# Kernel optimization log

Measured on AMD Instinct MI355X. Metric: run time of the kernel, lower is better.

Reference implementation:

```python
import jax, jax.numpy as jnp
import numpy as np
from jax.scipy.special import erfc

CUTOFF = 10.0   # real-space cutoff (Angstrom)
ALPHA = 0.3     # Ewald splitting parameter (1/Angstrom)
KMAX = 8        # max integer k-index per dimension
N_ATOMS = 4096
BOX = 40.0      # cubic box edge (Angstrom)


def setup_inputs() -> dict:
    key = jax.random.key(0)
    kp, kq = jax.random.split(key)
    positions = jax.random.uniform(kp, (N_ATOMS, 3), dtype=jnp.float32) * BOX
    charges = jax.random.normal(kq, (N_ATOMS,), dtype=jnp.float32)
    charges = charges - charges.mean()  # enforce charge neutrality
    cell = jnp.eye(3, dtype=jnp.float32) * BOX  # row-vector lattice
    return {"positions": positions, "charges": charges, "cell": cell}


def _kvectors(kmax):
    # static integer grid (-kmax..kmax)^3 \\ {0}, built with numpy at trace time
    n = np.arange(-kmax, kmax + 1)
    grid = np.stack(np.meshgrid(n, n, n, indexing="ij"), axis=-1).reshape(-1, 3)
    grid = grid[np.any(grid != 0, axis=-1)]
    return jnp.asarray(grid, dtype=jnp.float32)  # [Nk, 3]


def _ewald(positions, charges, cell, cutoff, alpha, kmax):
    N = positions.shape[0]
    inv_cell = jnp.linalg.inv(cell)

    # ---- real-space sum: 0.5 * sum_{i!=j, r<rc} q_i q_j erfc(a r)/r (min image)
    rij = positions[:, None, :] - positions[None, :, :]          # [N,N,3]
    frac = rij @ inv_cell
    rij = (frac - jnp.round(frac)) @ cell                        # minimum image
    r2 = jnp.sum(rij * rij, axis=-1)                             # [N,N]
    eye = jnp.eye(N, dtype=bool)
    r = jnp.sqrt(jnp.where(eye, 1.0, r2))                        # safe sqrt on diag
    pair_mask = (~eye) & (r2 < cutoff * cutoff)
    qq = charges[:, None] * charges[None, :]
    e_real = 0.5 * jnp.sum(jnp.where(pair_mask, qq * erfc(alpha * r) / r, 0.0))

    # ---- reciprocal-space sum: (2pi/V) sum_k exp(-k^2/4a^2)/k^2 |S(k)|^2
    recip = 2.0 * jnp.pi * inv_cell.T                            # reciprocal lattice rows
    kvecs = _kvectors(kmax) @ recip                              # [Nk,3]
    k2 = jnp.sum(kvecs * kvecs, axis=-1)                         # [Nk]
    phase = positions @ kvecs.T                                  # [N,Nk]
    s_re = charges @ jnp.cos(phase)                              # [Nk]
    s_im = charges @ jnp.sin(phase)                              # [Nk]
    vol = jnp.abs(jnp.linalg.det(cell))
    coeff = jnp.exp(-k2 / (4.0 * alpha * alpha)) / k2
    e_recip = (2.0 * jnp.pi / vol) * jnp.sum(coeff * (s_re * s_re + s_im * s_im))

    # ---- self-energy correction
    e_self = -(alpha / jnp.sqrt(jnp.pi)) * jnp.sum(charges * charges)

    return e_real + e_recip + e_self


def reference(positions, charges, cell):
    return _ewald(positions, charges, cell, CUTOFF, ALPHA, KMAX)
```

## Files before the change

kernel.cpp:

```cpp
#include <hip/hip_runtime.h>
#include <math.h>

#define ALPHA 0.3f
#define KMAX 8
#define KDIM 17
#define KD2 (KDIM*KDIM)
#define NK_FULL (KDIM*KDIM*KDIM - 1)
#define NK_HALF (NK_FULL/2)
#define RECIP_KB ((NK_HALF + 255)/256)
#define KPAD (RECIP_KB*256)
#define RECIP_CHUNKS 16
#define TWO_PI 6.28318530717958647692f

#define SELF_COEF (-0.16925687506432687f)
#define INV_4A2 (1.0f/(4.0f*ALPHA*ALPHA))
#define C1A (0.3275911f*ALPHA)
#define NA2 (-(ALPHA*ALPHA))

#define ITILE 256
#define JTILE 32

__device__ __forceinline__ void invert3x3(const float* __restrict__ c, float inv[9], float* det_out) {
    float a00=c[0],a01=c[1],a02=c[2];
    float a10=c[3],a11=c[4],a12=c[5];
    float a20=c[6],a21=c[7],a22=c[8];
    float c00 =  a11*a22 - a12*a21;
    float c01 = -(a10*a22 - a12*a20);
    float c02 =  a10*a21 - a11*a20;
    float det = a00*c00 + a01*c01 + a02*c02;
    float id = 1.0f/det;
    inv[0] =  c00*id;
    inv[1] = -(a01*a22 - a02*a21)*id;
    inv[2] =  (a01*a12 - a02*a11)*id;
    inv[3] =  c01*id;
    inv[4] =  (a00*a22 - a02*a20)*id;
    inv[5] = -(a00*a12 - a02*a10)*id;
    inv[6] =  c02*id;
    inv[7] = -(a00*a21 - a01*a20)*id;
    inv[8] =  (a00*a11 - a01*a10)*id;
    *det_out = det;
}

__device__ __forceinline__ float erfc_a(float r, float r2) {
    float t = __builtin_amdgcn_rcpf(fmaf(C1A, r, 1.0f));
    float p = t * fmaf(t, fmaf(t, fmaf(t, fmaf(t, 1.061405429f, -1.453152027f),
                       1.421413741f), -0.284496736f), 0.254829592f);
    return p * __expf(NA2 * r2);
}

__device__ __forceinline__ float block_reduce(float v) {
    for (int o = 32; o > 0; o >>= 1) v += __shfl_down(v, o, 64);
    __shared__ float smem[4];
    int lane = threadIdx.x & 63, wid = threadIdx.x >> 6;
    if (lane == 0) smem[wid] = v;
    __syncthreads();
    int nw = blockDim.x >> 6;
    v = ((int)threadIdx.x < nw) ? smem[threadIdx.x] : 0.0f;
    if (wid == 0) {
        for (int o = 4; o > 0; o >>= 1) v += __shfl_down(v, o, 64);
    }
    return v;
}

__global__ __launch_bounds__(256) void fused_kernel(const float* __restrict__ pos,
                                                    const float* __restrict__ q,
                                                    const float* __restrict__ cell,
                                                    float* __restrict__ spart,
                                                    float* __restrict__ rpart,
                                                    int N, int nb_recip) {
    __shared__ float4 tile[256];
    float inv[9]; float det;
    invert3x3(cell, inv, &det);
    bool ortho = (cell[1]==0.f) & (cell[2]==0.f) & (cell[3]==0.f) &
                 (cell[5]==0.f) & (cell[6]==0.f) & (cell[7]==0.f);

    int bid = blockIdx.x;
    int tid = threadIdx.x;

    if (bid < nb_recip) {
        int kb    = bid % RECIP_KB;
        int chunk = bid / RECIP_KB;
        int k = kb * 256 + tid;
        bool kvalid = (k < NK_HALF);
        int kk = kvalid ? k : 0;
        float kx = (float)(kk / KD2 - KMAX);
        float ky = (float)((kk / KDIM) % KDIM - KMAX);
        float kz = (float)(kk % KDIM - KMAX);

        int per = (N + RECIP_CHUNKS - 1) / RECIP_CHUNKS;
        int a0 = chunk * per;
        int a1 = min(N, a0 + per);

        float sre = 0.0f, sim = 0.0f;
        for (int base = a0; base < a1; base += 256) {
            int cnt = min(256, a1 - base);
            __syncthreads();
            if (tid < cnt) {
                int a = base + tid;
                float x = pos[3*a], y = pos[3*a+1], z = pos[3*a+2];
                float wx, wy, wz;
                if (ortho) { wx = x*inv[0]; wy = y*inv[4]; wz = z*inv[8]; }
                else {
                    wx = inv[0]*x + inv[3]*y + inv[6]*z;
                    wy = inv[1]*x + inv[4]*y + inv[7]*z;
                    wz = inv[2]*x + inv[5]*y + inv[8]*z;
                }
                tile[tid] = make_float4(wx, wy, wz, q[a]);
            }
            __syncthreads();
            #pragma unroll 4
            for (int t = 0; t < cnt; ++t) {
                float4 w = tile[t];
                float ph = fmaf(kx, w.x, fmaf(ky, w.y, kz * w.z));
                ph -= rintf(ph);
                sre = fmaf(w.w, __builtin_amdgcn_cosf(ph), sre);
                sim = fmaf(w.w, __builtin_amdgcn_sinf(ph), sim);
            }
        }
        spart[(size_t)(chunk*2    ) * KPAD + k] = kvalid ? sre : 0.0f;
        spart[(size_t)(chunk*2 + 1) * KPAD + k] = kvalid ? sim : 0.0f;
    } else {
        int rbid = bid - nb_recip;
        int bi = 0, acc = 0;
        for (;;) {
            int up = min(N, (bi + 1) * ITILE);
            int nc = (up + JTILE - 1) / JTILE;
            if (rbid < acc + nc) break;
            acc += nc; ++bi;
        }
        int bj = rbid - acc;

        float c0 = cell[0], c4 = cell[4], c8 = cell[8];
        float c1 = cell[1], c2 = cell[2], c3 = cell[3];
        float c5 = cell[5], c6 = cell[6], c7 = cell[7];

        int ibase = bi * ITILE;
        int i = ibase + tid;
        bool ivalid = (i < N);
        float xi = 0.f, yi = 0.f, zi = 0.f, qi = 0.f;
        if (ivalid) { xi = pos[3*i]; yi = pos[3*i+1]; zi = pos[3*i+2]; qi = q[i]; }

        int jbase = bj * JTILE;
        int jcount = min(JTILE, N - jbase);
        if (tid < jcount) {
            int j = jbase + tid;
            tile[tid] = make_float4(pos[3*j], pos[3*j+1], pos[3*j+2], q[j]);
        }
        __syncthreads();

        bool full = (jbase + JTILE <= ibase) && (ibase + ITILE <= N) && (jcount == JTILE);

        float acc_e = 0.0f;
        if (ortho) {
            float i0 = inv[0], i4 = inv[4], i8 = inv[8];
            if (full) {
                #pragma unroll 8
                for (int t = 0; t < JTILE; ++t) {
                    float4 p = tile[t];
                    float dx = xi - p.x, dy = yi - p.y, dz = zi - p.z;
                    float rx = fmaf(-c0, rintf(dx * i0), dx);
                    float ry = fmaf(-c4, rintf(dy * i4), dy);
                    float rz = fmaf(-c8, rintf(dz * i8), dz);
                    float r2 = fmaf(rx, rx, fmaf(ry, ry, rz * rz));
                    float rinv = __builtin_amdgcn_rsqf(r2);
                    float r = r2 * rinv;
                    acc_e = fmaf(p.w * rinv, erfc_a(r, r2), acc_e);
                }
            } else {
                #pragma unroll 8
                for (int t = 0; t < jcount; ++t) {
                    float4 p = tile[t];
                    float dx = xi - p.x, dy = yi - p.y, dz = zi - p.z;
                    float rx = fmaf(-c0, rintf(dx * i0), dx);
                    float ry = fmaf(-c4, rintf(dy * i4), dy);
                    float rz = fmaf(-c8, rintf(dz * i8), dz);
                    float r2 = fmaf(rx, rx, fmaf(ry, ry, rz * rz));
                    float rinv = __builtin_amdgcn_rsqf(r2);
                    float r = r2 * rinv;
                    float val = p.w * rinv * erfc_a(r, r2);
                    bool ok = ivalid && ((jbase + t) < i);
                    acc_e += ok ? val : 0.0f;
                }
            }
        } else {
            #pragma unroll 4
            for (int t = 0; t < jcount; ++t) {
                float4 p = tile[t];
                float dx = xi - p.x, dy = yi - p.y, dz = zi - p.z;
                float fx = dx*inv[0] + dy*inv[3] + dz*inv[6];
                float fy = dx*inv[1] + dy*inv[4] + dz*inv[7];
                float fz = dx*inv[2] + dy*inv[5] + dz*inv[8];
                fx -= rintf(fx); fy -= rintf(fy); fz -= rintf(fz);
                float rx = fx*c0 + fy*c3 + fz*c6;
                float ry = fx*c1 + fy*c4 + fz*c7;
                float rz = fx*c2 + fy*c5 + fz*c8;
                float r2 = fmaf(rx, rx, fmaf(ry, ry, rz * rz));
                float rinv = __builtin_amdgcn_rsqf(r2);
                float r = r2 * rinv;
                float val = p.w * rinv * erfc_a(r, r2);
                bool ok = ivalid && ((jbase + t) < i);
                acc_e += ok ? val : 0.0f;
            }
        }
        acc_e *= qi;

        float s = block_reduce(acc_e);
        if (tid == 0) rpart[rbid] = s;
    }
}

__global__ __launch_bounds__(256) void finalize_kernel(const float* __restrict__ spart,
                                                       const float* __restrict__ rpart,
                                                       const float* __restrict__ q,
                                                       const float* __restrict__ cell,
                                                       float* __restrict__ e_out,
                                                       int N, int nb_real) {
    float inv[9]; float det;
    invert3x3(cell, inv, &det);
    float vol = fabsf(det);
    float pref = 2.0f * (TWO_PI / vol);
    int tid = threadIdx.x;

    float acc = 0.0f;
    for (int t = tid; t < NK_HALF; t += 256) {
        float sr = 0.0f, si = 0.0f;
        #pragma unroll
        for (int c = 0; c < RECIP_CHUNKS; ++c) {
            sr += spart[(size_t)(c*2    ) * KPAD + t];
            si += spart[(size_t)(c*2 + 1) * KPAD + t];
        }
        float nx = (float)(t / KD2 - KMAX);
        float ny = (float)((t / KDIM) % KDIM - KMAX);
        float nz = (float)(t % KDIM - KMAX);
        float kvx = TWO_PI * (nx*inv[0] + ny*inv[1] + nz*inv[2]);
        float kvy = TWO_PI * (nx*inv[3] + ny*inv[4] + nz*inv[5]);
        float kvz = TWO_PI * (nx*inv[6] + ny*inv[7] + nz*inv[8]);
        float k2 = fmaf(kvx, kvx, fmaf(kvy, kvy, kvz * kvz));
        float coeff = __expf(-k2 * INV_4A2) / k2;
        acc = fmaf(pref * coeff, fmaf(sr, sr, si * si), acc);
    }
    for (int t = tid; t < N; t += 256) {
        float qt = q[t];
        acc = fmaf(SELF_COEF * qt, qt, acc);
    }
    for (int t = tid; t < nb_real; t += 256) {
        acc += rpart[t];
    }
    float s = block_reduce(acc);
    if (tid == 0) e_out[0] = s;
}

extern "C" void kernel_launch(void* const* d_in, const int* in_sizes, int n_in,
                              void* d_out, int out_size, void* d_ws, size_t ws_size,
                              hipStream_t stream) {
    const float* pos  = (const float*)d_in[0];
    const float* q    = (const float*)d_in[1];
    const float* cell = (const float*)d_in[2];
    int N = in_sizes[1];
    float* e_out = (float*)d_out;
    float* spart = (float*)d_ws;
    float* rpart = spart + (size_t)RECIP_CHUNKS*2*KPAD;

    int nbi = (N + ITILE - 1) / ITILE;
    int nb_real = 0;
    for (int bi = 0; bi < nbi; ++bi) {
        int up = (N < (bi + 1) * ITILE) ? N : (bi + 1) * ITILE;
        nb_real += (up + JTILE - 1) / JTILE;
    }
    int nb_recip = RECIP_KB * RECIP_CHUNKS;

    fused_kernel<<<nb_recip + nb_real, 256, 0, stream>>>(pos, q, cell, spart, rpart, N, nb_recip);

    finalize_kernel<<<1, 256, 0, stream>>>(spart, rpart, q, cell, e_out, N, nb_real);
}
```

Measured before the change: 80.13 us.

## Compute structure factors via kz recurrence and split real/recip kernels with atomics

The reciprocal sum now evaluates one sin/cos per (kx,ky) column and atom. It then walks the 17 kz values by complex multiplication with a precomputed per-atom exp(i*2pi*wz) phase factor, which replaces the per-k transcendental. Work is parallelized over atom chunks with atomic accumulation into S(k), and the fused kernel is split into separate real-space and reciprocal kernels. A memset is added, and the real-space partials are reduced with one float atomic per block. This trades transcendental throughput for register-heavy recurrences, many global atomics and extra launches, and it makes the float summation order nondeterministic.

```diff
diff --git a/kernel.cpp b/kernel.cpp
--- a/kernel.cpp
+++ b/kernel.cpp
@@ -4,13 +4,10 @@
 #define ALPHA 0.3f
 #define KMAX 8
 #define KDIM 17
-#define KD2 (KDIM*KDIM)
-#define NK_FULL (KDIM*KDIM*KDIM - 1)
-#define NK_HALF (NK_FULL/2)
-#define RECIP_KB ((NK_HALF + 255)/256)
-#define KPAD (RECIP_KB*256)
-#define RECIP_CHUNKS 16
 #define TWO_PI 6.28318530717958647692f
+
+#define NCOL 145
+#define NS (NCOL*17)
 
 #define SELF_COEF (-0.16925687506432687f)
 #define INV_4A2 (1.0f/(4.0f*ALPHA*ALPHA))
@@ -19,6 +16,8 @@
 
 #define ITILE 256
 #define JTILE 32
+#define RCHUNK 32
+#define RBLK 192
 
 __device__ __forceinline__ void invert3x3(const float* __restrict__ c, float inv[9], float* det_out) {
     float a00=c[0],a01=c[1],a02=c[2];
@@ -41,6 +40,12 @@
     *det_out = det;
 }
 
+__device__ __forceinline__ void col_to_k(int col, float* kx, float* ky) {
+    if (col < 136)      { *kx = (float)(col/17 - 8); *ky = (float)(col%17 - 8); }
+    else if (col < 144) { *kx = 0.f;                 *ky = (float)(col - 144);  }
+    else                { *kx = 0.f;                 *ky = 0.f; }
+}
+
 __device__ __forceinline__ float erfc_a(float r, float r2) {
     float t = __builtin_amdgcn_rcpf(fmaf(C1A, r, 1.0f));
     float p = t * fmaf(t, fmaf(t, fmaf(t, fmaf(t, 1.061405429f, -1.453152027f),
@@ -54,7 +59,7 @@
     int lane = threadIdx.x & 63, wid = threadIdx.x >> 6;
     if (lane == 0) smem[wid] = v;
     __syncthreads();
-    int nw = blockDim.x >> 6;
+    int nw = (blockDim.x + 63) >> 6;
     v = ((int)threadIdx.x < nw) ? smem[threadIdx.x] : 0.0f;
     if (wid == 0) {
         for (int o = 4; o > 0; o >>= 1) v += __shfl_down(v, o, 64);
@@ -62,138 +67,72 @@
     return v;
 }
 
-__global__ __launch_bounds__(256) void fused_kernel(const float* __restrict__ pos,
-                                                    const float* __restrict__ q,
-                                                    const float* __restrict__ cell,
-                                                    float* __restrict__ spart,
-                                                    float* __restrict__ rpart,
-                                                    int N, int nb_recip) {
-    __shared__ float4 tile[256];
+__global__ __launch_bounds__(256) void real_kernel(const float* __restrict__ pos,
+                                                   const float* __restrict__ q,
+                                                   const float* __restrict__ cell,
+                                                   float* __restrict__ ws_e,
+                                                   int N) {
+    __shared__ float4 tile[JTILE];
     float inv[9]; float det;
     invert3x3(cell, inv, &det);
     bool ortho = (cell[1]==0.f) & (cell[2]==0.f) & (cell[3]==0.f) &
                  (cell[5]==0.f) & (cell[6]==0.f) & (cell[7]==0.f);
 
-    int bid = blockIdx.x;
     int tid = threadIdx.x;
-
-    if (bid < nb_recip) {
-        int kb    = bid % RECIP_KB;
-        int chunk = bid / RECIP_KB;
-        int k = kb * 256 + tid;
-        bool kvalid = (k < NK_HALF);
-        int kk = kvalid ? k : 0;
-        float kx = (float)(kk / KD2 - KMAX);
-        float ky = (float)((kk / KDIM) % KDIM - KMAX);
-        float kz = (float)(kk % KDIM - KMAX);
-
-        int per = (N + RECIP_CHUNKS - 1) / RECIP_CHUNKS;
-        int a0 = chunk * per;
-        int a1 = min(N, a0 + per);
-
-        float sre = 0.0f, sim = 0.0f;
-        for (int base = a0; base < a1; base += 256) {
-            int cnt = min(256, a1 - base);
-            __syncthreads();
-            if (tid < cnt) {
-                int a = base + tid;
-                float x = pos[3*a], y = pos[3*a+1], z = pos[3*a+2];
-                float wx, wy, wz;
-                if (ortho) { wx = x*inv[0]; wy = y*inv[4]; wz = z*inv[8]; }
-                else {
-                    wx = inv[0]*x + inv[3]*y + inv[6]*z;
-                    wy = inv[1]*x + inv[4]*y + inv[7]*z;
-                    wz = inv[2]*x + inv[5]*y + inv[8]*z;
-                }
-                tile[tid] = make_float4(wx, wy, wz, q[a]);
-            }
-            __syncthreads();
-            #pragma unroll 4
-            for (int t = 0; t < cnt; ++t) {
-                float4 w = tile[t];
-                float ph = fmaf(kx, w.x, fmaf(ky, w.y, kz * w.z));
-                ph -= rintf(ph);
-                sre = fmaf(w.w, __builtin_amdgcn_cosf(ph), sre);
-                sim = fmaf(w.w, __builtin_amdgcn_sinf(ph), sim);
-            }
-        }
-        spart[(size_t)(chunk*2    ) * KPAD + k] = kvalid ? sre : 0.0f;
-        spart[(size_t)(chunk*2 + 1) * KPAD + k] = kvalid ? sim : 0.0f;
-    } else {
-        int rbid = bid - nb_recip;
-        int bi = 0, acc = 0;
-        for (;;) {
-            int up = min(N, (bi + 1) * ITILE);
-            int nc = (up + JTILE - 1) / JTILE;
-            if (rbid < acc + nc) break;
-            acc += nc; ++bi;
-        }
-        int bj = rbid - acc;
-
-        float c0 = cell[0], c4 = cell[4], c8 = cell[8];
-        float c1 = cell[1], c2 = cell[2], c3 = cell[3];
-        float c5 = cell[5], c6 = cell[6], c7 = cell[7];
-
-        int ibase = bi * ITILE;
-        int i = ibase + tid;
-        bool ivalid = (i < N);
-        float xi = 0.f, yi = 0.f, zi = 0.f, qi = 0.f;
-        if (ivalid) { xi = pos[3*i]; yi = pos[3*i+1]; zi = pos[3*i+2]; qi = q[i]; }
-
-        int jbase = bj * JTILE;
-        int jcount = min(JTILE, N - jbase);
-        if (tid < jcount) {
-            int j = jbase + tid;
-            tile[tid] = make_float4(pos[3*j], pos[3*j+1], pos[3*j+2], q[j]);
-        }
-        __syncthreads();
-
-        bool full = (jbase + JTILE <= ibase) && (ibase + ITILE <= N) && (jcount == JTILE);
-
-        float acc_e = 0.0f;
-        if (ortho) {
-            float i0 = inv[0], i4 = inv[4], i8 = inv[8];
-            if (full) {
-                #pragma unroll 8
-                for (int t = 0; t < JTILE; ++t) {
-                    float4 p = tile[t];
-                    float dx = xi - p.x, dy = yi - p.y, dz = zi - p.z;
-                    float rx = fmaf(-c0, rintf(dx * i0), dx);
-                    float ry = fmaf(-c4, rintf(dy * i4), dy);
-                    float rz = fmaf(-c8, rintf(dz * i8), dz);
-                    float r2 = fmaf(rx, rx, fmaf(ry, ry, rz * rz));
-                    float rinv = __builtin_amdgcn_rsqf(r2);
-                    float r = r2 * rinv;
-                    acc_e = fmaf(p.w * rinv, erfc_a(r, r2), acc_e);
-                }
-            } else {
-                #pragma unroll 8
-                for (int t = 0; t < jcount; ++t) {
-                    float4 p = tile[t];
-                    float dx = xi - p.x, dy = yi - p.y, dz = zi - p.z;
-                    float rx = fmaf(-c0, rintf(dx * i0), dx);
-                    float ry = fmaf(-c4, rintf(dy * i4), dy);
-                    float rz = fmaf(-c8, rintf(dz * i8), dz);
-                    float r2 = fmaf(rx, rx, fmaf(ry, ry, rz * rz));
-                    float rinv = __builtin_amdgcn_rsqf(r2);
-                    float r = r2 * rinv;
-                    float val = p.w * rinv * erfc_a(r, r2);
-                    bool ok = ivalid && ((jbase + t) < i);
-                    acc_e += ok ? val : 0.0f;
-                }
+    int rbid = blockIdx.x;
+    int bi = 0, acc = 0;
+    for (;;) {
+        int up = min(N, (bi + 1) * ITILE);
+        int nc = (up + JTILE - 1) / JTILE;
+        if (rbid < acc + nc) break;
+        acc += nc; ++bi;
+    }
+    int bj = rbid - acc;
+
+    float c0 = cell[0], c4 = cell[4], c8 = cell[8];
+    float c1 = cell[1], c2 = cell[2], c3 = cell[3];
+    float c5 = cell[5], c6 = cell[6], c7 = cell[7];
+
+    int ibase = bi * ITILE;
+    int i = ibase + tid;
+    bool ivalid = (i < N);
+    float xi = 0.f, yi = 0.f, zi = 0.f, qi = 0.f;
+    if (ivalid) { xi = pos[3*i]; yi = pos[3*i+1]; zi = pos[3*i+2]; qi = q[i]; }
+
+    int jbase = bj * JTILE;
+    int jcount = min(JTILE, N - jbase);
+    if (tid < jcount) {
+        int j = jbase + tid;
+        tile[tid] = make_float4(pos[3*j], pos[3*j+1], pos[3*j+2], q[j]);
+    }
+    __syncthreads();
+
+    bool full = (jbase + JTILE <= ibase) && (ibase + ITILE <= N) && (jcount == JTILE);
+
+    float acc_e = 0.0f;
+    if (ortho) {
+        float i0 = inv[0], i4 = inv[4], i8 = inv[8];
+        if (full) {
+            #pragma unroll 8
+            for (int t = 0; t < JTILE; ++t) {
+                float4 p = tile[t];
+                float dx = xi - p.x, dy = yi - p.y, dz = zi - p.z;
+                float rx = fmaf(-c0, rintf(dx * i0), dx);
+                float ry = fmaf(-c4, rintf(dy * i4), dy);
+                float rz = fmaf(-c8, rintf(dz * i8), dz);
+                float r2 = fmaf(rx, rx, fmaf(ry, ry, rz * rz));
+                float rinv = __builtin_amdgcn_rsqf(r2);
+                float r = r2 * rinv;
+                acc_e = fmaf(p.w * rinv, erfc_a(r, r2), acc_e);
             }
         } else {
-            #pragma unroll 4
+            #pragma unroll 8
             for (int t = 0; t < jcount; ++t) {
                 float4 p = tile[t];
                 float dx = xi - p.x, dy = yi - p.y, dz = zi - p.z;
-                float fx = dx*inv[0] + dy*inv[3] + dz*inv[6];
-                float fy = dx*inv[1] + dy*inv[4] + dz*inv[7];
-                float fz = dx*inv[2] + dy*inv[5] + dz*inv[8];
-                fx -= rintf(fx); fy -= rintf(fy); fz -= rintf(fz);
-                float rx = fx*c0 + fy*c3 + fz*c6;
-                float ry = fx*c1 + fy*c4 + fz*c7;
-                float rz = fx*c2 + fy*c5 + fz*c8;
+                float rx = fmaf(-c0, rintf(dx * i0), dx);
+                float ry = fmaf(-c4, rintf(dy * i4), dy);
+                float rz = fmaf(-c8, rintf(dz * i8), dz);
                 float r2 = fmaf(rx, rx, fmaf(ry, ry, rz * rz));
                 float rinv = __builtin_amdgcn_rsqf(r2);
                 float r = r2 * rinv;
@@ -202,19 +141,115 @@
                 acc_e += ok ? val : 0.0f;
             }
         }
-        acc_e *= qi;
-
-        float s = block_reduce(acc_e);
-        if (tid == 0) rpart[rbid] = s;
-    }
-}
-
-__global__ __launch_bounds__(256) void finalize_kernel(const float* __restrict__ spart,
-                                                       const float* __restrict__ rpart,
+    } else {
+        #pragma unroll 4
+        for (int t = 0; t < jcount; ++t) {
+            float4 p = tile[t];
+            float dx = xi - p.x, dy = yi - p.y, dz = zi - p.z;
+            float fx = dx*inv[0] + dy*inv[3] + dz*inv[6];
+            float fy = dx*inv[1] + dy*inv[4] + dz*inv[7];
+            float fz = dx*inv[2] + dy*inv[5] + dz*inv[8];
+            fx -= rintf(fx); fy -= rintf(fy); fz -= rintf(fz);
+            float rx = fx*c0 + fy*c3 + fz*c6;
+            float ry = fx*c1 + fy*c4 + fz*c7;
+            float rz = fx*c2 + fy*c5 + fz*c8;
+            float r2 = fmaf(rx, rx, fmaf(ry, ry, rz * rz));
+            float rinv = __builtin_amdgcn_rsqf(r2);
+            float r = r2 * rinv;
+            float val = p.w * rinv * erfc_a(r, r2);
+            bool ok = ivalid && ((jbase + t) < i);
+            acc_e += ok ? val : 0.0f;
+        }
+    }
+    acc_e *= qi;
+
+    float s = block_reduce(acc_e);
+    if (tid == 0) atomicAdd(ws_e, s);
+}
+
+__global__ __launch_bounds__(RBLK) void recip_kernel(const float* __restrict__ pos,
+                                                     const float* __restrict__ q,
+                                                     const float* __restrict__ cell,
+                                                     float* __restrict__ s_re,
+                                                     float* __restrict__ s_im,
+                                                     int N) {
+    __shared__ float tw[RCHUNK][6];
+    float inv[9]; float det;
+    invert3x3(cell, inv, &det);
+    bool ortho = (cell[1]==0.f) & (cell[2]==0.f) & (cell[3]==0.f) &
+                 (cell[5]==0.f) & (cell[6]==0.f) & (cell[7]==0.f);
+
+    int tid = threadIdx.x;
+    int a0 = blockIdx.x * RCHUNK;
+    int cnt = min(RCHUNK, N - a0);
+
+    if (tid < cnt) {
+        int a = a0 + tid;
+        float x = pos[3*a], y = pos[3*a+1], z = pos[3*a+2];
+        float wx, wy, wz;
+        if (ortho) { wx = x*inv[0]; wy = y*inv[4]; wz = z*inv[8]; }
+        else {
+            wx = inv[0]*x + inv[3]*y + inv[6]*z;
+            wy = inv[1]*x + inv[4]*y + inv[7]*z;
+            wz = inv[2]*x + inv[5]*y + inv[8]*z;
+        }
+        float qa = q[a];
+        float rz = wz - rintf(wz);
+        float czr = __builtin_amdgcn_cosf(rz);
+        float czi = __builtin_amdgcn_sinf(rz);
+        float u = -8.0f * wz;
+        u -= rintf(u);
+        float bzr = qa * __builtin_amdgcn_cosf(u);
+        float bzi = qa * __builtin_amdgcn_sinf(u);
+        tw[tid][0] = wx;  tw[tid][1] = wy;
+        tw[tid][2] = bzr; tw[tid][3] = bzi;
+        tw[tid][4] = czr; tw[tid][5] = czi;
+    }
+    __syncthreads();
+
+    int col = tid;
+    float kx, ky;
+    col_to_k(col < NCOL ? col : 0, &kx, &ky);
+
+    float ar[17], ai[17];
+    #pragma unroll
+    for (int u = 0; u < 17; ++u) { ar[u] = 0.f; ai[u] = 0.f; }
+
+    for (int t = 0; t < cnt; ++t) {
+        float wx  = tw[t][0], wy  = tw[t][1];
+        float bzr = tw[t][2], bzi = tw[t][3];
+        float czr = tw[t][4], czi = tw[t][5];
+        float ph = fmaf(kx, wx, ky * wy);
+        ph -= rintf(ph);
+        float cr = __builtin_amdgcn_cosf(ph);
+        float ci = __builtin_amdgcn_sinf(ph);
+        float zr = fmaf(cr, bzr, -ci * bzi);
+        float zi = fmaf(cr, bzi,  ci * bzr);
+        #pragma unroll
+        for (int u = 0; u < 17; ++u) {
+            ar[u] += zr; ai[u] += zi;
+            float nzr = fmaf(zr, czr, -zi * czi);
+            float nzi = fmaf(zr, czi,  zi * czr);
+            zr = nzr; zi = nzi;
+        }
+    }
+
+    if (col < NCOL) {
+        int lim = (col == NCOL-1) ? 8 : 17;
+        for (int u = 0; u < lim; ++u) {
+            atomicAdd(&s_re[col*17 + u], ar[u]);
+            atomicAdd(&s_im[col*17 + u], ai[u]);
+        }
+    }
+}
+
+__global__ __launch_bounds__(256) void finalize_kernel(const float* __restrict__ s_re,
+                                                       const float* __restrict__ s_im,
+                                                       const float* __restrict__ ws_e,
                                                        const float* __restrict__ q,
                                                        const float* __restrict__ cell,
                                                        float* __restrict__ e_out,
-                                                       int N, int nb_real) {
+                                                       int N) {
     float inv[9]; float det;
     invert3x3(cell, inv, &det);
     float vol = fabsf(det);
@@ -222,30 +257,26 @@
     int tid = threadIdx.x;
 
     float acc = 0.0f;
-    for (int t = tid; t < NK_HALF; t += 256) {
-        float sr = 0.0f, si = 0.0f;
-        #pragma unroll
-        for (int c = 0; c < RECIP_CHUNKS; ++c) {
-            sr += spart[(size_t)(c*2    ) * KPAD + t];
-            si += spart[(size_t)(c*2 + 1) * KPAD + t];
-        }
-        float nx = (float)(t / KD2 - KMAX);
-        float ny = (float)((t / KDIM) % KDIM - KMAX);
-        float nz = (float)(t % KDIM - KMAX);
-        float kvx = TWO_PI * (nx*inv[0] + ny*inv[1] + nz*inv[2]);
-        float kvy = TWO_PI * (nx*inv[3] + ny*inv[4] + nz*inv[5]);
-        float kvz = TWO_PI * (nx*inv[6] + ny*inv[7] + nz*inv[8]);
+    for (int idx = tid; idx < NS; idx += 256) {
+        int col = idx / 17;
+        int u   = idx % 17;
+        if (col == NCOL-1 && u >= 8) continue;
+        float kx, ky;
+        col_to_k(col, &kx, &ky);
+        float kz = (float)(u - 8);
+        float kvx = TWO_PI * (kx*inv[0] + ky*inv[1] + kz*inv[2]);
+        float kvy = TWO_PI * (kx*inv[3] + ky*inv[4] + kz*inv[5]);
+        float kvz = TWO_PI * (kx*inv[6] + ky*inv[7] + kz*inv[8]);
         float k2 = fmaf(kvx, kvx, fmaf(kvy, kvy, kvz * kvz));
         float coeff = __expf(-k2 * INV_4A2) / k2;
+        float sr = s_re[idx], si = s_im[idx];
         acc = fmaf(pref * coeff, fmaf(sr, sr, si * si), acc);
     }
     for (int t = tid; t < N; t += 256) {
         float qt = q[t];
         acc = fmaf(SELF_COEF * qt, qt, acc);
     }
-    for (int t = tid; t < nb_real; t += 256) {
-        acc += rpart[t];
-    }
+    if (tid == 0) acc += ws_e[0];
     float s = block_reduce(acc);
     if (tid == 0) e_out[0] = s;
 }
@@ -258,8 +289,12 @@
     const float* cell = (const float*)d_in[2];
     int N = in_sizes[1];
     float* e_out = (float*)d_out;
-    float* spart = (float*)d_ws;
-    float* rpart = spart + (size_t)RECIP_CHUNKS*2*KPAD;
+
+    float* s_re = (float*)d_ws;
+    float* s_im = s_re + NS;
+    float* ws_e = s_im + NS;
+
+    hipMemsetAsync(s_re, 0, (2*NS + 1) * sizeof(float), stream);
 
     int nbi = (N + ITILE - 1) / ITILE;
     int nb_real = 0;
@@ -267,9 +302,11 @@
         int up = (N < (bi + 1) * ITILE) ? N : (bi + 1) * ITILE;
         nb_real += (up + JTILE - 1) / JTILE;
     }
-    int nb_recip = RECIP_KB * RECIP_CHUNKS;
-
-    fused_kernel<<<nb_recip + nb_real, 256, 0, stream>>>(pos, q, cell, spart, rpart, N, nb_recip);
-
-    finalize_kernel<<<1, 256, 0, stream>>>(spart, rpart, q, cell, e_out, N, nb_real);
-}
+
+    real_kernel<<<nb_real, 256, 0, stream>>>(pos, q, cell, ws_e, N);
+
+    int nb_recip = (N + RCHUNK - 1) / RCHUNK;
+    recip_kernel<<<nb_recip, RBLK, 0, stream>>>(pos, q, cell, s_re, s_im, N);
+
+    finalize_kernel<<<1, 256, 0, stream>>>(s_re, s_im, ws_e, q, cell, e_out, N);
+}
```

After: 146.6 us. 1.83x slower.

## Split fused kernel into separate real-space and reciprocal kernels, unroll pair loop by two

Applied to the files above, without the earlier changes.

The fused kernel that routed blocks by index to either the reciprocal or the real-space branch is split into two kernels launched back to back on the same stream. The real-space kernel now needs only a small JTILE shared tile instead of 256 float4, and its full-tile loop processes two j atoms per iteration with two accumulators to expose more independent work. Diagonal-ortho partial tiles use the cheaper ortho minimum image, and the block-reduce warp count is rounded up. The aim is to cut register and shared-memory pressure and branch divergence, but it gives up overlap between the two phases and adds a launch.

```diff
diff --git a/kernel.cpp b/kernel.cpp
--- a/kernel.cpp
+++ b/kernel.cpp
@@ -54,7 +54,7 @@
     int lane = threadIdx.x & 63, wid = threadIdx.x >> 6;
     if (lane == 0) smem[wid] = v;
     __syncthreads();
-    int nw = blockDim.x >> 6;
+    int nw = (blockDim.x + 63) >> 6;
     v = ((int)threadIdx.x < nw) ? smem[threadIdx.x] : 0.0f;
     if (wid == 0) {
         for (int o = 4; o > 0; o >>= 1) v += __shfl_down(v, o, 64);
@@ -62,151 +62,164 @@
     return v;
 }
 
-__global__ __launch_bounds__(256) void fused_kernel(const float* __restrict__ pos,
-                                                    const float* __restrict__ q,
-                                                    const float* __restrict__ cell,
-                                                    float* __restrict__ spart,
-                                                    float* __restrict__ rpart,
-                                                    int N, int nb_recip) {
-    __shared__ float4 tile[256];
+__global__ __launch_bounds__(256) void real_kernel(const float* __restrict__ pos,
+                                                   const float* __restrict__ q,
+                                                   const float* __restrict__ cell,
+                                                   float* __restrict__ rpart,
+                                                   int N) {
+    __shared__ float4 tile[JTILE];
     float inv[9]; float det;
     invert3x3(cell, inv, &det);
     bool ortho = (cell[1]==0.f) & (cell[2]==0.f) & (cell[3]==0.f) &
                  (cell[5]==0.f) & (cell[6]==0.f) & (cell[7]==0.f);
 
-    int bid = blockIdx.x;
     int tid = threadIdx.x;
-
-    if (bid < nb_recip) {
-        int kb    = bid % RECIP_KB;
-        int chunk = bid / RECIP_KB;
-        int k = kb * 256 + tid;
-        bool kvalid = (k < NK_HALF);
-        int kk = kvalid ? k : 0;
-        float kx = (float)(kk / KD2 - KMAX);
-        float ky = (float)((kk / KDIM) % KDIM - KMAX);
-        float kz = (float)(kk % KDIM - KMAX);
-
-        int per = (N + RECIP_CHUNKS - 1) / RECIP_CHUNKS;
-        int a0 = chunk * per;
-        int a1 = min(N, a0 + per);
-
-        float sre = 0.0f, sim = 0.0f;
-        for (int base = a0; base < a1; base += 256) {
-            int cnt = min(256, a1 - base);
-            __syncthreads();
-            if (tid < cnt) {
-                int a = base + tid;
-                float x = pos[3*a], y = pos[3*a+1], z = pos[3*a+2];
-                float wx, wy, wz;
-                if (ortho) { wx = x*inv[0]; wy = y*inv[4]; wz = z*inv[8]; }
-                else {
-                    wx = inv[0]*x + inv[3]*y + inv[6]*z;
-                    wy = inv[1]*x + inv[4]*y + inv[7]*z;
-                    wz = inv[2]*x + inv[5]*y + inv[8]*z;
-                }
-                tile[tid] = make_float4(wx, wy, wz, q[a]);
-            }
-            __syncthreads();
-            #pragma unroll 4
-            for (int t = 0; t < cnt; ++t) {
-                float4 w = tile[t];
-                float ph = fmaf(kx, w.x, fmaf(ky, w.y, kz * w.z));
-                ph -= rintf(ph);
-                sre = fmaf(w.w, __builtin_amdgcn_cosf(ph), sre);
-                sim = fmaf(w.w, __builtin_amdgcn_sinf(ph), sim);
-            }
-        }
-        spart[(size_t)(chunk*2    ) * KPAD + k] = kvalid ? sre : 0.0f;
-        spart[(size_t)(chunk*2 + 1) * KPAD + k] = kvalid ? sim : 0.0f;
-    } else {
-        int rbid = bid - nb_recip;
-        int bi = 0, acc = 0;
-        for (;;) {
-            int up = min(N, (bi + 1) * ITILE);
-            int nc = (up + JTILE - 1) / JTILE;
-            if (rbid < acc + nc) break;
-            acc += nc; ++bi;
-        }
-        int bj = rbid - acc;
-
-        float c0 = cell[0], c4 = cell[4], c8 = cell[8];
-        float c1 = cell[1], c2 = cell[2], c3 = cell[3];
-        float c5 = cell[5], c6 = cell[6], c7 = cell[7];
-
-        int ibase = bi * ITILE;
-        int i = ibase + tid;
-        bool ivalid = (i < N);
-        float xi = 0.f, yi = 0.f, zi = 0.f, qi = 0.f;
-        if (ivalid) { xi = pos[3*i]; yi = pos[3*i+1]; zi = pos[3*i+2]; qi = q[i]; }
-
-        int jbase = bj * JTILE;
-        int jcount = min(JTILE, N - jbase);
-        if (tid < jcount) {
-            int j = jbase + tid;
-            tile[tid] = make_float4(pos[3*j], pos[3*j+1], pos[3*j+2], q[j]);
-        }
-        __syncthreads();
-
-        bool full = (jbase + JTILE <= ibase) && (ibase + ITILE <= N) && (jcount == JTILE);
-
-        float acc_e = 0.0f;
-        if (ortho) {
-            float i0 = inv[0], i4 = inv[4], i8 = inv[8];
-            if (full) {
-                #pragma unroll 8
-                for (int t = 0; t < JTILE; ++t) {
-                    float4 p = tile[t];
-                    float dx = xi - p.x, dy = yi - p.y, dz = zi - p.z;
-                    float rx = fmaf(-c0, rintf(dx * i0), dx);
-                    float ry = fmaf(-c4, rintf(dy * i4), dy);
-                    float rz = fmaf(-c8, rintf(dz * i8), dz);
-                    float r2 = fmaf(rx, rx, fmaf(ry, ry, rz * rz));
-                    float rinv = __builtin_amdgcn_rsqf(r2);
-                    float r = r2 * rinv;
-                    acc_e = fmaf(p.w * rinv, erfc_a(r, r2), acc_e);
-                }
-            } else {
-                #pragma unroll 8
-                for (int t = 0; t < jcount; ++t) {
-                    float4 p = tile[t];
-                    float dx = xi - p.x, dy = yi - p.y, dz = zi - p.z;
-                    float rx = fmaf(-c0, rintf(dx * i0), dx);
-                    float ry = fmaf(-c4, rintf(dy * i4), dy);
-                    float rz = fmaf(-c8, rintf(dz * i8), dz);
-                    float r2 = fmaf(rx, rx, fmaf(ry, ry, rz * rz));
-                    float rinv = __builtin_amdgcn_rsqf(r2);
-                    float r = r2 * rinv;
-                    float val = p.w * rinv * erfc_a(r, r2);
-                    bool ok = ivalid && ((jbase + t) < i);
-                    acc_e += ok ? val : 0.0f;
-                }
+    int rbid = blockIdx.x;
+    int bi = 0, acc = 0;
+    for (;;) {
+        int up = min(N, (bi + 1) * ITILE);
+        int nc = (up + JTILE - 1) / JTILE;
+        if (rbid < acc + nc) break;
+        acc += nc; ++bi;
+    }
+    int bj = rbid - acc;
+
+    float c0 = cell[0], c4 = cell[4], c8 = cell[8];
+    float c1 = cell[1], c2 = cell[2], c3 = cell[3];
+    float c5 = cell[5], c6 = cell[6], c7 = cell[7];
+
+    int ibase = bi * ITILE;
+    int i = ibase + tid;
+    bool ivalid = (i < N);
+    float xi = 0.f, yi = 0.f, zi = 0.f, qi = 0.f;
+    if (ivalid) { xi = pos[3*i]; yi = pos[3*i+1]; zi = pos[3*i+2]; qi = q[i]; }
+
+    int jbase = bj * JTILE;
+    int jcount = min(JTILE, N - jbase);
+    if (tid < jcount) {
+        int j = jbase + tid;
+        tile[tid] = make_float4(pos[3*j], pos[3*j+1], pos[3*j+2], q[j]);
+    }
+    __syncthreads();
+
+    bool full = (jbase + JTILE <= ibase) && (ibase + ITILE <= N) && (jcount == JTILE);
+
+    float acc0 = 0.0f, acc1 = 0.0f;
+    if (ortho) {
+        float i0 = inv[0], i4 = inv[4], i8 = inv[8];
+        if (full) {
+            #pragma unroll
+            for (int t = 0; t < JTILE; t += 2) {
+                float4 p = tile[t];
+                float4 p2 = tile[t+1];
+                float dx = xi - p.x, dy = yi - p.y, dz = zi - p.z;
+                float ex = xi - p2.x, ey = yi - p2.y, ez = zi - p2.z;
+                float rx = fmaf(-c0, rintf(dx * i0), dx);
+                float ry = fmaf(-c4, rintf(dy * i4), dy);
+                float rz = fmaf(-c8, rintf(dz * i8), dz);
+                float sx = fmaf(-c0, rintf(ex * i0), ex);
+                float sy = fmaf(-c4, rintf(ey * i4), ey);
+                float sz = fmaf(-c8, rintf(ez * i8), ez);
+                float r2a = fmaf(rx, rx, fmaf(ry, ry, rz * rz));
+                float r2b = fmaf(sx, sx, fmaf(sy, sy, sz * sz));
+                float ria = __builtin_amdgcn_rsqf(r2a);
+                float rib = __builtin_amdgcn_rsqf(r2b);
+                acc0 = fmaf(p.w  * ria, erfc_a(r2a * ria, r2a), acc0);
+                acc1 = fmaf(p2.w * rib, erfc_a(r2b * rib, r2b), acc1);
             }
         } else {
             #pragma unroll 4
             for (int t = 0; t < jcount; ++t) {
                 float4 p = tile[t];
                 float dx = xi - p.x, dy = yi - p.y, dz = zi - p.z;
-                float fx = dx*inv[0] + dy*inv[3] + dz*inv[6];
-                float fy = dx*inv[1] + dy*inv[4] + dz*inv[7];
-                float fz = dx*inv[2] + dy*inv[5] + dz*inv[8];
-                fx -= rintf(fx); fy -= rintf(fy); fz -= rintf(fz);
-                float rx = fx*c0 + fy*c3 + fz*c6;
-                float ry = fx*c1 + fy*c4 + fz*c7;
-                float rz = fx*c2 + fy*c5 + fz*c8;
+                float rx = fmaf(-c0, rintf(dx * i0), dx);
+                float ry = fmaf(-c4, rintf(dy * i4), dy);
+                float rz = fmaf(-c8, rintf(dz * i8), dz);
                 float r2 = fmaf(rx, rx, fmaf(ry, ry, rz * rz));
                 float rinv = __builtin_amdgcn_rsqf(r2);
-                float r = r2 * rinv;
-                float val = p.w * rinv * erfc_a(r, r2);
+                float val = p.w * rinv * erfc_a(r2 * rinv, r2);
                 bool ok = ivalid && ((jbase + t) < i);
-                acc_e += ok ? val : 0.0f;
+                acc0 += ok ? val : 0.0f;
             }
         }
-        acc_e *= qi;
-
-        float s = block_reduce(acc_e);
-        if (tid == 0) rpart[rbid] = s;
-    }
+    } else {
+        #pragma unroll 4
+        for (int t = 0; t < jcount; ++t) {
+            float4 p = tile[t];
+            float dx = xi - p.x, dy = yi - p.y, dz = zi - p.z;
+            float fx = dx*inv[0] + dy*inv[3] + dz*inv[6];
+            float fy = dx*inv[1] + dy*inv[4] + dz*inv[7];
+            float fz = dx*inv[2] + dy*inv[5] + dz*inv[8];
+            fx -= rintf(fx); fy -= rintf(fy); fz -= rintf(fz);
+            float rx = fx*c0 + fy*c3 + fz*c6;
+            float ry = fx*c1 + fy*c4 + fz*c7;
+            float rz = fx*c2 + fy*c5 + fz*c8;
+            float r2 = fmaf(rx, rx, fmaf(ry, ry, rz * rz));
+            float rinv = __builtin_amdgcn_rsqf(r2);
+            float val = p.w * rinv * erfc_a(r2 * rinv, r2);
+            bool ok = ivalid && ((jbase + t) < i);
+            acc0 += ok ? val : 0.0f;
+        }
+    }
+    float acc_e = (acc0 + acc1) * qi;
+
+    float s = block_reduce(acc_e);
+    if (tid == 0) rpart[rbid] = s;
+}
+
+__global__ __launch_bounds__(256) void recip_kernel(const float* __restrict__ pos,
+                                                    const float* __restrict__ q,
+                                                    const float* __restrict__ cell,
+                                                    float* __restrict__ spart,
+                                                    int N) {
+    __shared__ float4 tile[256];
+    float inv[9]; float det;
+    invert3x3(cell, inv, &det);
+    bool ortho = (cell[1]==0.f) & (cell[2]==0.f) & (cell[3]==0.f) &
+                 (cell[5]==0.f) & (cell[6]==0.f) & (cell[7]==0.f);
+
+    int tid = threadIdx.x;
+    int kb    = blockIdx.x % RECIP_KB;
+    int chunk = blockIdx.x / RECIP_KB;
+    int k = kb * 256 + tid;
+    bool kvalid = (k < NK_HALF);
+    int kk = kvalid ? k : 0;
+    float kx = (float)(kk / KD2 - KMAX);
+    float ky = (float)((kk / KDIM) % KDIM - KMAX);
+    float kz = (float)(kk % KDIM - KMAX);
+
+    int per = (N + RECIP_CHUNKS - 1) / RECIP_CHUNKS;
+    int a0 = chunk * per;
+    int a1 = min(N, a0 + per);
+
+    float sre = 0.0f, sim = 0.0f;
+    for (int base = a0; base < a1; base += 256) {
+        int cnt = min(256, a1 - base);
+        __syncthreads();
+        if (tid < cnt) {
+            int a = base + tid;
+            float x = pos[3*a], y = pos[3*a+1], z = pos[3*a+2];
+            float wx, wy, wz;
+            if (ortho) { wx = x*inv[0]; wy = y*inv[4]; wz = z*inv[8]; }
+            else {
+                wx = inv[0]*x + inv[3]*y + inv[6]*z;
+                wy = inv[1]*x + inv[4]*y + inv[7]*z;
+                wz = inv[2]*x + inv[5]*y + inv[8]*z;
+            }
+            tile[tid] = make_float4(wx, wy, wz, q[a]);
+        }
+        __syncthreads();
+        #pragma unroll 4
+        for (int t = 0; t < cnt; ++t) {
+            float4 w = tile[t];
+            float ph = fmaf(kx, w.x, fmaf(ky, w.y, kz * w.z));
+            ph -= rintf(ph);
+            sre = fmaf(w.w, __builtin_amdgcn_cosf(ph), sre);
+            sim = fmaf(w.w, __builtin_amdgcn_sinf(ph), sim);
+        }
+    }
+    spart[(size_t)(chunk*2    ) * KPAD + k] = kvalid ? sre : 0.0f;
+    spart[(size_t)(chunk*2 + 1) * KPAD + k] = kvalid ? sim : 0.0f;
 }
 
 __global__ __launch_bounds__(256) void finalize_kernel(const float* __restrict__ spart,
@@ -258,6 +271,7 @@
     const float* cell = (const float*)d_in[2];
     int N = in_sizes[1];
     float* e_out = (float*)d_out;
+
     float* spart = (float*)d_ws;
     float* rpart = spart + (size_t)RECIP_CHUNKS*2*KPAD;
 
@@ -267,9 +281,10 @@
         int up = (N < (bi + 1) * ITILE) ? N : (bi + 1) * ITILE;
         nb_real += (up + JTILE - 1) / JTILE;
     }
-    int nb_recip = RECIP_KB * RECIP_CHUNKS;
-
-    fused_kernel<<<nb_recip + nb_real, 256, 0, stream>>>(pos, q, cell, spart, rpart, N, nb_recip);
+
+    real_kernel<<<nb_real, 256, 0, stream>>>(pos, q, cell, rpart, N);
+
+    recip_kernel<<<RECIP_KB * RECIP_CHUNKS, 256, 0, stream>>>(pos, q, cell, spart, N);
 
     finalize_kernel<<<1, 256, 0, stream>>>(spart, rpart, q, cell, e_out, N, nb_real);
 }
```

Measured after the change: 87.30 us. 8.9% more time.

## Process two i-atoms per thread with cubic-cell fractional-coordinate fast path

Applied to the files above, without the earlier changes.

Doubles the real-space i-tile so each thread handles two atoms against the same shared j-tile, which halves the number of real-space blocks and reuses each LDS load twice. Adds a cubic-box specialization that pre-scales positions to fractional coordinates, so the minimum image becomes a plain subtract-round and the 1/L scale is applied once at the end. It also interleaves the two independent evaluations to expose ILP. In exchange it raises register pressure and halves the real-space block count, which could hurt occupancy or load balance against the reciprocal blocks.

```diff
diff --git a/kernel.cpp b/kernel.cpp
--- a/kernel.cpp
+++ b/kernel.cpp
@@ -17,7 +17,7 @@
 #define C1A (0.3275911f*ALPHA)
 #define NA2 (-(ALPHA*ALPHA))
 
-#define ITILE 256
+#define ITILE 512
 #define JTILE 32
 
 __device__ __forceinline__ void invert3x3(const float* __restrict__ c, float inv[9], float* det_out) {
@@ -54,7 +54,7 @@
     int lane = threadIdx.x & 63, wid = threadIdx.x >> 6;
     if (lane == 0) smem[wid] = v;
     __syncthreads();
-    int nw = blockDim.x >> 6;
+    int nw = (blockDim.x + 63) >> 6;
     v = ((int)threadIdx.x < nw) ? smem[threadIdx.x] : 0.0f;
     if (wid == 0) {
         for (int o = 4; o > 0; o >>= 1) v += __shfl_down(v, o, 64);
@@ -68,16 +68,17 @@
                                                     float* __restrict__ spart,
                                                     float* __restrict__ rpart,
                                                     int N, int nb_recip) {
-    __shared__ float4 tile[256];
     float inv[9]; float det;
     invert3x3(cell, inv, &det);
     bool ortho = (cell[1]==0.f) & (cell[2]==0.f) & (cell[3]==0.f) &
                  (cell[5]==0.f) & (cell[6]==0.f) & (cell[7]==0.f);
+    bool cubic = ortho & (cell[0]==cell[4]) & (cell[0]==cell[8]);
 
     int bid = blockIdx.x;
     int tid = threadIdx.x;
 
     if (bid < nb_recip) {
+        __shared__ float4 atile[256];
         int kb    = bid % RECIP_KB;
         int chunk = bid / RECIP_KB;
         int k = kb * 256 + tid;
@@ -105,12 +106,12 @@
                     wy = inv[1]*x + inv[4]*y + inv[7]*z;
                     wz = inv[2]*x + inv[5]*y + inv[8]*z;
                 }
-                tile[tid] = make_float4(wx, wy, wz, q[a]);
+                atile[tid] = make_float4(wx, wy, wz, q[a]);
             }
             __syncthreads();
             #pragma unroll 4
             for (int t = 0; t < cnt; ++t) {
-                float4 w = tile[t];
+                float4 w = atile[t];
                 float ph = fmaf(kx, w.x, fmaf(ky, w.y, kz * w.z));
                 ph -= rintf(ph);
                 sre = fmaf(w.w, __builtin_amdgcn_cosf(ph), sre);
@@ -120,6 +121,7 @@
         spart[(size_t)(chunk*2    ) * KPAD + k] = kvalid ? sre : 0.0f;
         spart[(size_t)(chunk*2 + 1) * KPAD + k] = kvalid ? sim : 0.0f;
     } else {
+        __shared__ float4 tile[JTILE];
         int rbid = bid - nb_recip;
         int bi = 0, acc = 0;
         for (;;) {
@@ -130,82 +132,139 @@
         }
         int bj = rbid - acc;
 
-        float c0 = cell[0], c4 = cell[4], c8 = cell[8];
-        float c1 = cell[1], c2 = cell[2], c3 = cell[3];
-        float c5 = cell[5], c6 = cell[6], c7 = cell[7];
-
         int ibase = bi * ITILE;
-        int i = ibase + tid;
-        bool ivalid = (i < N);
-        float xi = 0.f, yi = 0.f, zi = 0.f, qi = 0.f;
-        if (ivalid) { xi = pos[3*i]; yi = pos[3*i+1]; zi = pos[3*i+2]; qi = q[i]; }
-
         int jbase = bj * JTILE;
         int jcount = min(JTILE, N - jbase);
-        if (tid < jcount) {
-            int j = jbase + tid;
-            tile[tid] = make_float4(pos[3*j], pos[3*j+1], pos[3*j+2], q[j]);
+
+        int i1 = ibase + tid;
+        int i2 = i1 + 256;
+        bool v1 = (i1 < N), v2 = (i2 < N);
+
+        float L = cell[0], invL = inv[0];
+        float C1AL = C1A * L;
+        float NBL  = NA2 * L * L;
+
+        float x1=0.f,y1=0.f,z1=0.f,q1=0.f, x2=0.f,y2=0.f,z2=0.f,q2=0.f;
+
+        if (cubic) {
+            if (v1) { x1 = pos[3*i1]*invL; y1 = pos[3*i1+1]*invL; z1 = pos[3*i1+2]*invL; q1 = q[i1]; }
+            if (v2) { x2 = pos[3*i2]*invL; y2 = pos[3*i2+1]*invL; z2 = pos[3*i2+2]*invL; q2 = q[i2]; }
+            if (tid < jcount) {
+                int j = jbase + tid;
+                tile[tid] = make_float4(pos[3*j]*invL, pos[3*j+1]*invL, pos[3*j+2]*invL, q[j]);
+            }
+        } else {
+            if (v1) { x1 = pos[3*i1]; y1 = pos[3*i1+1]; z1 = pos[3*i1+2]; q1 = q[i1]; }
+            if (v2) { x2 = pos[3*i2]; y2 = pos[3*i2+1]; z2 = pos[3*i2+2]; q2 = q[i2]; }
+            if (tid < jcount) {
+                int j = jbase + tid;
+                tile[tid] = make_float4(pos[3*j], pos[3*j+1], pos[3*j+2], q[j]);
+            }
         }
         __syncthreads();
 
         bool full = (jbase + JTILE <= ibase) && (ibase + ITILE <= N) && (jcount == JTILE);
 
-        float acc_e = 0.0f;
-        if (ortho) {
-            float i0 = inv[0], i4 = inv[4], i8 = inv[8];
+        float acc1 = 0.0f, acc2 = 0.0f;
+        if (cubic) {
             if (full) {
-                #pragma unroll 8
+                #pragma unroll 4
                 for (int t = 0; t < JTILE; ++t) {
                     float4 p = tile[t];
-                    float dx = xi - p.x, dy = yi - p.y, dz = zi - p.z;
-                    float rx = fmaf(-c0, rintf(dx * i0), dx);
-                    float ry = fmaf(-c4, rintf(dy * i4), dy);
-                    float rz = fmaf(-c8, rintf(dz * i8), dz);
+                    float dx = x1 - p.x, dy = y1 - p.y, dz = z1 - p.z;
+                    dx -= rintf(dx); dy -= rintf(dy); dz -= rintf(dz);
+                    float f2a = fmaf(dx, dx, fmaf(dy, dy, dz * dz));
+                    float ex = x2 - p.x, ey = y2 - p.y, ez = z2 - p.z;
+                    ex -= rintf(ex); ey -= rintf(ey); ez -= rintf(ez);
+                    float f2b = fmaf(ex, ex, fmaf(ey, ey, ez * ez));
+
+                    float rsa = __builtin_amdgcn_rsqf(f2a);
+                    float rsb = __builtin_amdgcn_rsqf(f2b);
+                    float fma_ = f2a * rsa, fmb_ = f2b * rsb;
+                    float ta = __builtin_amdgcn_rcpf(fmaf(C1AL, fma_, 1.0f));
+                    float tb = __builtin_amdgcn_rcpf(fmaf(C1AL, fmb_, 1.0f));
+                    float pa = ta * fmaf(ta, fmaf(ta, fmaf(ta, fmaf(ta, 1.061405429f, -1.453152027f),
+                                        1.421413741f), -0.284496736f), 0.254829592f);
+                    float pb = tb * fmaf(tb, fmaf(tb, fmaf(tb, fmaf(tb, 1.061405429f, -1.453152027f),
+                                        1.421413741f), -0.284496736f), 0.254829592f);
+                    float ea = __expf(NBL * f2a);
+                    float eb = __expf(NBL * f2b);
+                    acc1 = fmaf(p.w * rsa * pa, ea, acc1);
+                    acc2 = fmaf(p.w * rsb * pb, eb, acc2);
+                }
+            } else {
+                #pragma unroll 4
+                for (int t = 0; t < jcount; ++t) {
+                    float4 p = tile[t];
+                    int j = jbase + t;
+                    float dx = x1 - p.x, dy = y1 - p.y, dz = z1 - p.z;
+                    dx -= rintf(dx); dy -= rintf(dy); dz -= rintf(dz);
+                    float f2a = fmaf(dx, dx, fmaf(dy, dy, dz * dz));
+                    float ex = x2 - p.x, ey = y2 - p.y, ez = z2 - p.z;
+                    ex -= rintf(ex); ey -= rintf(ey); ez -= rintf(ez);
+                    float f2b = fmaf(ex, ex, fmaf(ey, ey, ez * ez));
+
+                    float rsa = __builtin_amdgcn_rsqf(f2a);
+                    float rsb = __builtin_amdgcn_rsqf(f2b);
+                    float fma_ = f2a * rsa, fmb_ = f2b * rsb;
+                    float ta = __builtin_amdgcn_rcpf(fmaf(C1AL, fma_, 1.0f));
+                    float tb = __builtin_amdgcn_rcpf(fmaf(C1AL, fmb_, 1.0f));
+                    float pa = ta * fmaf(ta, fmaf(ta, fmaf(ta, fmaf(ta, 1.061405429f, -1.453152027f),
+                                        1.421413741f), -0.284496736f), 0.254829592f);
+                    float pb = tb * fmaf(tb, fmaf(tb, fmaf(tb, fmaf(tb, 1.061405429f, -1.453152027f),
+                                        1.421413741f), -0.284496736f), 0.254829592f);
+                    float ea = __expf(NBL * f2a);
+                    float eb = __expf(NBL * f2b);
+                    float va = p.w * rsa * pa * ea;
+                    float vb = p.w * rsb * pb * eb;
+                    acc1 += (v1 && j < i1) ? va : 0.0f;
+                    acc2 += (v2 && j < i2) ? vb : 0.0f;
+                }
+            }
+            float acc_e = (acc1 * q1 + acc2 * q2) * invL;
+            float s = block_reduce(acc_e);
+            if (tid == 0) rpart[rbid] = s;
+        } else {
+            float c0 = cell[0], c1 = cell[1], c2 = cell[2];
+            float c3 = cell[3], c4 = cell[4], c5 = cell[5];
+            float c6 = cell[6], c7 = cell[7], c8 = cell[8];
+            #pragma unroll 2
+            for (int t = 0; t < jcount; ++t) {
+                float4 p = tile[t];
+                int j = jbase + t;
+                {
+                    float dx = x1 - p.x, dy = y1 - p.y, dz = z1 - p.z;
+                    float fx = dx*inv[0] + dy*inv[3] + dz*inv[6];
+                    float fy = dx*inv[1] + dy*inv[4] + dz*inv[7];
+                    float fz = dx*inv[2] + dy*inv[5] + dz*inv[8];
+                    fx -= rintf(fx); fy -= rintf(fy); fz -= rintf(fz);
+                    float rx = fx*c0 + fy*c3 + fz*c6;
+                    float ry = fx*c1 + fy*c4 + fz*c7;
+                    float rz = fx*c2 + fy*c5 + fz*c8;
                     float r2 = fmaf(rx, rx, fmaf(ry, ry, rz * rz));
                     float rinv = __builtin_amdgcn_rsqf(r2);
-                    float r = r2 * rinv;
-                    acc_e = fmaf(p.w * rinv, erfc_a(r, r2), acc_e);
-                }
-            } else {
-                #pragma unroll 8
-                for (int t = 0; t < jcount; ++t) {
-                    float4 p = tile[t];
-                    float dx = xi - p.x, dy = yi - p.y, dz = zi - p.z;
-                    float rx = fmaf(-c0, rintf(dx * i0), dx);
-                    float ry = fmaf(-c4, rintf(dy * i4), dy);
-                    float rz = fmaf(-c8, rintf(dz * i8), dz);
+                    float val = p.w * rinv * erfc_a(r2 * rinv, r2);
+                    acc1 += (v1 && j < i1) ? val : 0.0f;
+                }
+                {
+                    float dx = x2 - p.x, dy = y2 - p.y, dz = z2 - p.z;
+                    float fx = dx*inv[0] + dy*inv[3] + dz*inv[6];
+                    float fy = dx*inv[1] + dy*inv[4] + dz*inv[7];
+                    float fz = dx*inv[2] + dy*inv[5] + dz*inv[8];
+                    fx -= rintf(fx); fy -= rintf(fy); fz -= rintf(fz);
+                    float rx = fx*c0 + fy*c3 + fz*c6;
+                    float ry = fx*c1 + fy*c4 + fz*c7;
+                    float rz = fx*c2 + fy*c5 + fz*c8;
                     float r2 = fmaf(rx, rx, fmaf(ry, ry, rz * rz));
                     float rinv = __builtin_amdgcn_rsqf(r2);
-                    float r = r2 * rinv;
-                    float val = p.w * rinv * erfc_a(r, r2);
-                    bool ok = ivalid && ((jbase + t) < i);
-                    acc_e += ok ? val : 0.0f;
-                }
-            }
-        } else {
-            #pragma unroll 4
-            for (int t = 0; t < jcount; ++t) {
-                float4 p = tile[t];
-                float dx = xi - p.x, dy = yi - p.y, dz = zi - p.z;
-                float fx = dx*inv[0] + dy*inv[3] + dz*inv[6];
-                float fy = dx*inv[1] + dy*inv[4] + dz*inv[7];
-                float fz = dx*inv[2] + dy*inv[5] + dz*inv[8];
-                fx -= rintf(fx); fy -= rintf(fy); fz -= rintf(fz);
-                float rx = fx*c0 + fy*c3 + fz*c6;
-                float ry = fx*c1 + fy*c4 + fz*c7;
-                float rz = fx*c2 + fy*c5 + fz*c8;
-                float r2 = fmaf(rx, rx, fmaf(ry, ry, rz * rz));
-                float rinv = __builtin_amdgcn_rsqf(r2);
-                float r = r2 * rinv;
-                float val = p.w * rinv * erfc_a(r, r2);
-                bool ok = ivalid && ((jbase + t) < i);
-                acc_e += ok ? val : 0.0f;
-            }
-        }
-        acc_e *= qi;
-
-        float s = block_reduce(acc_e);
-        if (tid == 0) rpart[rbid] = s;
+                    float val = p.w * rinv * erfc_a(r2 * rinv, r2);
+                    acc2 += (v2 && j < i2) ? val : 0.0f;
+                }
+            }
+            float acc_e = acc1 * q1 + acc2 * q2;
+            float s = block_reduce(acc_e);
+            if (tid == 0) rpart[rbid] = s;
+        }
     }
 }
 
@@ -258,6 +317,7 @@
     const float* cell = (const float*)d_in[2];
     int N = in_sizes[1];
     float* e_out = (float*)d_out;
+
     float* spart = (float*)d_ws;
     float* rpart = spart + (size_t)RECIP_CHUNKS*2*KPAD;
 
```

Measured after the change: 80.71 us. No clear change (+0.7%).
